# Kernel tuning notes

Measured on AMD Instinct MI355X. Metric: run time of the kernel, lower is better.

## Reference

```python
import jax, jax.numpy as jnp
import numpy as np
import math

B, S, H = 4, 1024, 1024
NH, DH = 16, 64  # MULTI_HEAD, HIDDEN_SIZE_HEAD


def setup_inputs() -> dict:
    key = jax.random.key(0)
    ks = jax.random.split(key, 14)
    w = lambda k: (jax.random.normal(k, (H, H), dtype=jnp.float32) * 0.02)
    b = lambda k: (jax.random.normal(k, (H,), dtype=jnp.float32) * 0.02)
    return {
        "v": jax.random.normal(ks[0], (B, S, H), dtype=jnp.float32),
        "k": jax.random.normal(ks[1], (B, S, H), dtype=jnp.float32),
        "q": jax.random.normal(ks[2], (B, S, H), dtype=jnp.float32),
        "mask": jax.random.randint(ks[3], (B, 1, 1, S), 0, 2) == 1,
        "group_prob": jax.random.uniform(ks[4], (B, S, S), dtype=jnp.float32),
        "Wq": w(ks[5]), "bq": b(ks[6]),
        "Wk": w(ks[7]), "bk": b(ks[8]),
        "Wv": w(ks[9]), "bv": b(ks[10]),
        "Wm": w(ks[11]), "bm": b(ks[12]),
    }


def reference(v, k, q, mask, group_prob, Wq, bq, Wk, bk, Wv, bv, Wm, bm):
    nb = q.shape[0]
    inv_sqrt_dk = 1.0 / math.sqrt(DH)

    def proj(x, W, b):
        # torch Linear: x @ W.T + b, then split heads -> [B, NH, S, DH]
        y = jnp.einsum('bsh,oh->bso', x, W) + b
        return y.reshape(nb, -1, NH, DH).transpose(0, 2, 1, 3)

    qh = proj(q, Wq, bq)
    kh = proj(k, Wk, bk)
    vh = proj(v, Wv, bv)

    scores = jnp.einsum('bhqd,bhkd->bhqk', qh, kh) * inv_sqrt_dk
    scores = jnp.where(mask, jnp.float32(-1e9), scores)
    att = jax.nn.softmax(scores, axis=-1)
    # post-softmax group-prior scaling (the non-standard part)
    att = att * group_prob[:, None, :, :]
    # dropout in eval mode = identity
    out = jnp.einsum('bhqk,bhkd->bhqd', att, vh)
    out = out.transpose(0, 2, 1, 3).reshape(nb, -1, H)
    return jnp.einsum('bsh,oh->bso', out, Wm) + bm
```

## Files before the change

### kernel.cpp

```cpp
#include <hip/hip_runtime.h>

#define S_LEN 1024
#define NHEAD 16
#define DHEAD 64

typedef _Float16 half8 __attribute__((ext_vector_type(8)));
typedef _Float16 half4v __attribute__((ext_vector_type(4)));
typedef float floatx4 __attribute__((ext_vector_type(4)));

#define QSCALE 0.125f
#define EXPSHIFT 4.0f

__device__ __forceinline__ void gll16(const _Float16* g, _Float16* s) {
    __builtin_amdgcn_global_load_lds(
        (const __attribute__((address_space(1))) void*)g,
        (__attribute__((address_space(3))) void*)s, 16, 0, 0);
}

struct SplitArgs {
    const float* src[7];
    _Float16* hi[7];
    int nblk[7];
};

__global__ __launch_bounds__(256) void split_all_kernel(SplitArgs a)
{
    int blk = blockIdx.x, seg = 0, off = 0;
    while (blk >= off + a.nblk[seg]) { off += a.nblk[seg]; ++seg; }
    const int base = (blk - off) * 4096 + threadIdx.x * 4;
#pragma unroll
    for (int u = 0; u < 4; ++u) {
        const int i = base + u * 1024;
        float4 v = *(const float4*)&a.src[seg][i];
        half4v h;
        h.x = (_Float16)v.x; h.y = (_Float16)v.y;
        h.z = (_Float16)v.z; h.w = (_Float16)v.w;
        *(half4v*)&a.hi[seg][i] = h;
    }
}

__global__ __launch_bounds__(256) void gp_prep_kernel(
    const float* __restrict__ gp, _Float16* __restrict__ gpt)
{
    __shared__ _Float16 G[128 * 64];
    const int t = threadIdx.x;
    const int tile = blockIdx.x;
    const int kt = tile & 15, qt = (tile >> 4) & 7, b = tile >> 7;
    const float* src = gp + ((size_t)(b * S_LEN + qt * 128)) * S_LEN + kt * 64;

#pragma unroll
    for (int it = 0; it < 8; ++it) {
        const int idx = it * 256 + t;
        const int q = idx >> 4, kk = (idx & 15) * 4;
        float4 v = *(const float4*)&src[(size_t)q * S_LEN + kk];
        half4v h;
        h.x = (_Float16)v.x; h.y = (_Float16)v.y;
        h.z = (_Float16)v.z; h.w = (_Float16)v.w;
        *(half4v*)&G[q * 64 + kk] = h;
    }
    __syncthreads();

    _Float16* dst = gpt + (size_t)tile * 8192;
#pragma unroll
    for (int ph = 0; ph < 4; ++ph) {
        const int chunk = ph * 256 + t;
        const int l = chunk & 63;
        const int rest = chunk >> 6;
        const int h2 = rest & 1, mt = (rest >> 1) & 1, w = rest >> 2;
        const int qb = w * 32 + mt * 16 + (l >> 4) * 4;
        const int kb = l & 15;
        half8 o;
#pragma unroll
        for (int jj = 0; jj < 2; ++jj)
#pragma unroll
            for (int rg = 0; rg < 4; ++rg)
                o[jj * 4 + rg] = G[(qb + rg) * 64 + kb + (h2 * 2 + jj) * 16];
        *(half8*)&dst[chunk * 8] = o;
    }
}

struct ProjArgs {
    const _Float16* A[3];
    const _Float16* B[3];
    const float* bias[3];
    _Float16* C[3];
};

__global__ __launch_bounds__(256, 3) void proj_gemm_kernel(ProjArgs p)
{
    __shared__ __align__(16) _Float16 Ab[128 * 64];
    __shared__ __align__(16) _Float16 Bb[128 * 64];

    const int bid = blockIdx.x;
    const int xcd = bid & 7;
    const int slot = bid >> 3;
    const int mg = slot & 3;
    const int bx = (slot >> 2) & 7;
    const int z  = slot >> 5;
    const int by = xcd + mg * 8;

    const _Float16* A = p.A[z];
    const _Float16* B = p.B[z];
    const float* bias = p.bias[z];
    _Float16* C = p.C[z];

    const int t = threadIdx.x;
    const int w = t >> 6;
    const int l = t & 63;
    const int r = l & 15;
    const int quad = l >> 4;
    const int k7 = r & 7;
    const int rr = l >> 3, ii = l & 7;
    const int wm = (w >> 1) * 64, wn = (w & 1) * 64;
    const int m0 = by * 128;
    const int n0 = bx * 128;

    floatx4 acc[4][4];
#pragma unroll
    for (int i = 0; i < 4; ++i)
#pragma unroll
        for (int j = 0; j < 4; ++j) acc[i][j] = (floatx4){0.f, 0.f, 0.f, 0.f};

    const _Float16* ssrc = (w < 2) ? A : B;
    _Float16* sdst = (w < 2) ? Ab : Bb;
    const int srow0 = (w < 2) ? m0 : n0;
    const int w01 = w & 1;

    auto stage = [&](int kt) {
        const int k0 = kt * 64;
#pragma unroll
        for (int c = 0; c < 8; ++c) {
            const int R = w01 * 64 + c * 8 + rr;
            const int j = ii ^ (R & 7);
            gll16(ssrc + (size_t)(srow0 + R) * 1024 + k0 + j * 8,
                  sdst + R * 64 + ii * 8);
        }
    };

    stage(0);
    for (int kt = 0; kt < 16; ++kt) {
        __syncthreads();

        half8 ah[4][2], bh[4][2];
#pragma unroll
        for (int i = 0; i < 4; ++i) {
            const int R = wm + i * 16 + r;
            ah[i][0] = *(const half8*)&Ab[R * 64 + ((quad ^ k7) << 3)];
            ah[i][1] = *(const half8*)&Ab[R * 64 + (((4 | quad) ^ k7) << 3)];
        }
#pragma unroll
        for (int j = 0; j < 4; ++j) {
            const int R = wn + j * 16 + r;
            bh[j][0] = *(const half8*)&Bb[R * 64 + ((quad ^ k7) << 3)];
            bh[j][1] = *(const half8*)&Bb[R * 64 + (((4 | quad) ^ k7) << 3)];
        }
        __syncthreads();

        if (kt + 1 < 16) stage(kt + 1);

#pragma unroll
        for (int c = 0; c < 2; ++c)
#pragma unroll
            for (int i = 0; i < 4; ++i)
#pragma unroll
                for (int j = 0; j < 4; ++j)
                    acc[i][j] = __builtin_amdgcn_mfma_f32_16x16x32_f16(
                        ah[i][c], bh[j][c], acc[i][j], 0, 0, 0);
    }

#pragma unroll
    for (int i = 0; i < 4; ++i)
#pragma unroll
        for (int j = 0; j < 4; ++j) {
            const int n = n0 + wn + j * 16 + r;
            const float bv = bias[n];
#pragma unroll
            for (int reg = 0; reg < 4; ++reg) {
                const int m = m0 + wm + i * 16 + quad * 4 + reg;
                float val = acc[i][j][reg] + bv;
                if (z == 0) val *= QSCALE;
                const int b = m >> 10, s = m & 1023;
                const int h = n >> 6, d = n & 63;
                const size_t idx = (z == 2)
                    ? (((size_t)(b * NHEAD + h)) * DHEAD + d) * S_LEN + s
                    : (((size_t)(b * NHEAD + h)) * S_LEN + s) * DHEAD + d;
                C[idx] = (_Float16)val;
            }
        }
}

__global__ __launch_bounds__(256, 2) void out_gemm_kernel(
    const _Float16* __restrict__ A, const _Float16* __restrict__ B,
    const float* __restrict__ bias, float* __restrict__ C)
{
    __shared__ __align__(16) _Float16 Ab[128 * 64];
    __shared__ __align__(16) _Float16 Bb[64 * 64];

    const int bid = blockIdx.x;
    const int xcd = bid & 7;
    const int slot = bid >> 3;
    const int by = xcd + (slot & 3) * 8;
    const int bx = slot >> 2;

    const int t = threadIdx.x;
    const int w = t >> 6;
    const int l = t & 63;
    const int r = l & 15;
    const int quad = l >> 4;
    const int k7 = r & 7;
    const int rr = l >> 3, ii = l & 7;
    const int m0 = by * 128, n0 = bx * 64;

    floatx4 acc[2][4];
#pragma unroll
    for (int mt = 0; mt < 2; ++mt)
#pragma unroll
        for (int j = 0; j < 4; ++j) acc[mt][j] = (floatx4){0.f, 0.f, 0.f, 0.f};

    auto stage = [&](int kt) {
        const int k0 = kt * 64;
        if (w < 2) {
#pragma unroll
            for (int c = 0; c < 8; ++c) {
                const int R = (w & 1) * 64 + c * 8 + rr;
                const int j = ii ^ (R & 7);
                gll16(A + (size_t)(m0 + R) * 1024 + k0 + j * 8,
                      Ab + R * 64 + ii * 8);
            }
        } else {
#pragma unroll
            for (int c = 0; c < 4; ++c) {
                const int R = (w - 2) * 32 + c * 8 + rr;
                const int j = ii ^ (R & 7);
                gll16(B + (size_t)(n0 + R) * 1024 + k0 + j * 8,
                      Bb + R * 64 + ii * 8);
            }
        }
    };

    stage(0);
    for (int kt = 0; kt < 16; ++kt) {
        __syncthreads();

        half8 ah[2][2], bh[4][2];
#pragma unroll
        for (int mt = 0; mt < 2; ++mt) {
            const int R = w * 32 + mt * 16 + r;
            ah[mt][0] = *(const half8*)&Ab[R * 64 + ((quad ^ k7) << 3)];
            ah[mt][1] = *(const half8*)&Ab[R * 64 + (((4 | quad) ^ k7) << 3)];
        }
#pragma unroll
        for (int j = 0; j < 4; ++j) {
            const int R = j * 16 + r;
            bh[j][0] = *(const half8*)&Bb[R * 64 + ((quad ^ k7) << 3)];
            bh[j][1] = *(const half8*)&Bb[R * 64 + (((4 | quad) ^ k7) << 3)];
        }
        __syncthreads();

        if (kt + 1 < 16) stage(kt + 1);

#pragma unroll
        for (int c = 0; c < 2; ++c)
#pragma unroll
            for (int mt = 0; mt < 2; ++mt)
#pragma unroll
                for (int j = 0; j < 4; ++j)
                    acc[mt][j] = __builtin_amdgcn_mfma_f32_16x16x32_f16(
                        ah[mt][c], bh[j][c], acc[mt][j], 0, 0, 0);
    }

#pragma unroll
    for (int mt = 0; mt < 2; ++mt)
#pragma unroll
        for (int j = 0; j < 4; ++j) {
            const int n = n0 + j * 16 + r;
            const float bv = bias[n];
#pragma unroll
            for (int reg = 0; reg < 4; ++reg) {
                const int m = m0 + w * 32 + mt * 16 + quad * 4 + reg;
                C[(size_t)m * 1024 + n] = acc[mt][j][reg] + bv;
            }
        }
}

__global__ __launch_bounds__(256, 2) void attention_mfma_kernel(
    const _Float16* __restrict__ Qhi, const _Float16* __restrict__ Khi,
    const _Float16* __restrict__ Vthi, const _Float16* __restrict__ gpt,
    const int* __restrict__ mask, _Float16* __restrict__ OutHi)
{
    __shared__ __align__(16) _Float16 KhS[2][4096];
    __shared__ __align__(16) _Float16 VhS[2][4096];
    __shared__ __align__(16) _Float16 PS[8192];
    __shared__ int maskS[1024];

    const int t = threadIdx.x;
    const int w = t >> 6;
    const int l = t & 63;
    const int lr = l & 15;
    const int quad = l >> 4;
    const int rr = l >> 3;
    const int ii = l & 7;

    const int h  = blockIdx.x & 15;
    const int qt = (blockIdx.x >> 4) & 7;
    const int b  = blockIdx.x >> 7;
    const int q0 = qt * 128;
    const size_t hb = (size_t)(b * NHEAD + h) * (S_LEN * DHEAD);
    const _Float16* gptile = gpt + (size_t)((b * 8 + qt) * 16) * 8192;

    ((int4*)maskS)[t] = ((const int4*)(mask + (size_t)b * S_LEN))[t];

    half8 qfh[2][2];
#pragma unroll
    for (int mt = 0; mt < 2; ++mt)
#pragma unroll
        for (int c = 0; c < 2; ++c) {
            const size_t off = hb + (size_t)(q0 + w * 32 + mt * 16 + lr) * 64 + c * 32 + quad * 8;
            qfh[mt][c] = *(const half8*)&Qhi[off];
        }

    float lpart[2][4];
    floatx4 Oa[2][4];
#pragma unroll
    for (int mt = 0; mt < 2; ++mt)
#pragma unroll
        for (int rg = 0; rg < 4; ++rg) {
            lpart[mt][rg] = 0.0f;
            Oa[mt][rg] = (floatx4){0.f, 0.f, 0.f, 0.f};
        }

    auto stageK = [&](int kt, int bf) {
        const int k0n = kt * 64;
#pragma unroll
        for (int c2 = 0; c2 < 2; ++c2) {
            const int c = w * 2 + c2;
            const int row = c * 8 + rr;
            const int j = ii ^ (row & 7);
            gll16(Khi + hb + (size_t)(k0n + row) * 64 + j * 8,
                  &KhS[bf][0] + c * 512 + l * 8);
        }
    };
    auto stageV = [&](int kt, int bf) {
        const int k0n = kt * 64;
#pragma unroll
        for (int c2 = 0; c2 < 2; ++c2) {
            const int i = w * 2 + c2;
            const int row = i * 8 + rr;
            const int j = ii ^ (row & 7);
            gll16(Vthi + hb + (size_t)row * S_LEN + k0n + j * 8,
                  &VhS[bf][0] + i * 512 + l * 8);
        }
    };
    auto loadG = [&](half8 (&g)[2][2], int kt) {
#pragma unroll
        for (int mt = 0; mt < 2; ++mt)
#pragma unroll
            for (int h2 = 0; h2 < 2; ++h2)
                g[mt][h2] = *(const half8*)&gptile[(size_t)kt * 8192 +
                    (((w * 2 + mt) * 2 + h2) * 64 + l) * 8];
    };

    half8 gc[2][2], gn[2][2];
    stageK(0, 0);
    stageV(0, 0);
    loadG(gc, 0);
    __syncthreads();

    for (int kt = 0; kt < 16; ++kt) {
        const int bf = kt & 1;
        const int k0 = kt * 64;

        if (kt + 1 < 16) {
            stageK(kt + 1, bf ^ 1);
            stageV(kt + 1, bf ^ 1);
            loadG(gn, kt + 1);
        }

        int mk[4];
#pragma unroll
        for (int j = 0; j < 4; ++j) mk[j] = maskS[k0 + j * 16 + lr];

        floatx4 sc[2][4];
#pragma unroll
        for (int mt = 0; mt < 2; ++mt)
#pragma unroll
            for (int j = 0; j < 4; ++j) sc[mt][j] = (floatx4){0.f, 0.f, 0.f, 0.f};

#pragma unroll
        for (int j = 0; j < 4; ++j) {
            const int key = j * 16 + lr;
            const int base = key * 64;
            const int k7a = key & 7;
            const half8 kh0 = *(const half8*)&KhS[bf][base + (quad ^ k7a) * 8];
            const half8 kh1 = *(const half8*)&KhS[bf][base + ((4 + quad) ^ k7a) * 8];
#pragma unroll
            for (int mt = 0; mt < 2; ++mt) {
                floatx4 a = sc[mt][j];
                a = __builtin_amdgcn_mfma_f32_16x16x32_f16(qfh[mt][0], kh0, a, 0, 0, 0);
                a = __builtin_amdgcn_mfma_f32_16x16x32_f16(qfh[mt][1], kh1, a, 0, 0, 0);
                sc[mt][j] = a;
            }
        }

#pragma unroll
        for (int mt = 0; mt < 2; ++mt) {
            const half8 g0 = gc[mt][0];
            const half8 g1 = gc[mt][1];
            const int qlb = w * 32 + mt * 16 + quad * 4;
#pragma unroll
            for (int j = 0; j < 4; ++j) {
                const int col = j * 16 + lr;
                const int cc = col >> 3, wi = col & 7;
#pragma unroll
                for (int rg = 0; rg < 4; ++rg) {
                    const float p = mk[j] ? 0.0f : __expf(sc[mt][j][rg] - EXPSHIFT);
                    lpart[mt][rg] += p;
                    const float g = (float)((j < 2) ? g0[(j & 1) * 4 + rg]
                                                    : g1[(j & 1) * 4 + rg]);
                    const int qloc = qlb + rg;
                    PS[qloc * 64 + (cc ^ (qloc & 7)) * 8 + wi] = (_Float16)(p * g);
                }
            }
        }

        half8 pf[2][2];
#pragma unroll
        for (int mt = 0; mt < 2; ++mt) {
            const int qloc = w * 32 + mt * 16 + lr;
            const int q7 = qloc & 7;
            pf[mt][0] = *(const half8*)&PS[qloc * 64 + (quad ^ q7) * 8];
            pf[mt][1] = *(const half8*)&PS[qloc * 64 + ((4 + quad) ^ q7) * 8];
        }
#pragma unroll
        for (int dt = 0; dt < 4; ++dt) {
            const int d = dt * 16 + lr;
            const int base = d * 64, d7 = d & 7;
            const half8 vh0 = *(const half8*)&VhS[bf][base + (quad ^ d7) * 8];
            const half8 vh1 = *(const half8*)&VhS[bf][base + ((4 + quad) ^ d7) * 8];
#pragma unroll
            for (int mt = 0; mt < 2; ++mt) {
                floatx4 a = Oa[mt][dt];
                a = __builtin_amdgcn_mfma_f32_16x16x32_f16(pf[mt][0], vh0, a, 0, 0, 0);
                a = __builtin_amdgcn_mfma_f32_16x16x32_f16(pf[mt][1], vh1, a, 0, 0, 0);
                Oa[mt][dt] = a;
            }
        }

        __syncthreads();

        if (kt + 1 < 16) {
#pragma unroll
            for (int mt = 0; mt < 2; ++mt)
#pragma unroll
                for (int h2 = 0; h2 < 2; ++h2) gc[mt][h2] = gn[mt][h2];
        }
    }

#pragma unroll
    for (int mt = 0; mt < 2; ++mt)
#pragma unroll
        for (int rg = 0; rg < 4; ++rg) {
#pragma unroll
            for (int off = 1; off < 16; off <<= 1)
                lpart[mt][rg] += __shfl_xor(lpart[mt][rg], off, 64);
        }

#pragma unroll
    for (int mt = 0; mt < 2; ++mt)
#pragma unroll
        for (int rg = 0; rg < 4; ++rg) {
            const int s = q0 + w * 32 + mt * 16 + quad * 4 + rg;
            const float linv = 1.0f / lpart[mt][rg];
#pragma unroll
            for (int dt = 0; dt < 4; ++dt) {
                const float val = Oa[mt][dt][rg] * linv;
                const size_t idx = ((size_t)(b * S_LEN + s)) * 1024 + h * 64 + dt * 16 + lr;
                OutHi[idx] = (_Float16)val;
            }
        }
}

extern "C" void kernel_launch(void* const* d_in, const int* in_sizes, int n_in,
                              void* d_out, int out_size, void* d_ws, size_t ws_size,
                              hipStream_t stream) {
    const float* v    = (const float*)d_in[0];
    const float* k    = (const float*)d_in[1];
    const float* q    = (const float*)d_in[2];
    const int*   mask = (const int*)d_in[3];
    const float* gp   = (const float*)d_in[4];
    const float* Wq   = (const float*)d_in[5];
    const float* bq   = (const float*)d_in[6];
    const float* Wk   = (const float*)d_in[7];
    const float* bk   = (const float*)d_in[8];
    const float* Wv   = (const float*)d_in[9];
    const float* bv   = (const float*)d_in[10];
    const float* Wm   = (const float*)d_in[11];
    const float* bm   = (const float*)d_in[12];
    float* out = (float*)d_out;

    uint8_t* w8 = (uint8_t*)d_ws;
    const size_t MB = 1024 * 1024;
    _Float16* q_h  = (_Float16*)(w8 + 0 * MB);
    _Float16* k_h  = (_Float16*)(w8 + 8 * MB);
    _Float16* v_h  = (_Float16*)(w8 + 16 * MB);
    _Float16* Wq_h = (_Float16*)(w8 + 24 * MB);
    _Float16* Wk_h = (_Float16*)(w8 + 26 * MB);
    _Float16* Wv_h = (_Float16*)(w8 + 28 * MB);
    _Float16* Wm_h = (_Float16*)(w8 + 30 * MB);
    _Float16* Qh   = (_Float16*)(w8 + 32 * MB);
    _Float16* Kh   = (_Float16*)(w8 + 40 * MB);
    _Float16* Vt   = (_Float16*)(w8 + 48 * MB);
    _Float16* gpt  = (_Float16*)(w8 + 56 * MB);
    _Float16* at   = (_Float16*)(w8 + 0 * MB);

    SplitArgs sa;
    sa.src[0] = q;  sa.hi[0] = q_h;  sa.nblk[0] = 1024;
    sa.src[1] = k;  sa.hi[1] = k_h;  sa.nblk[1] = 1024;
    sa.src[2] = v;  sa.hi[2] = v_h;  sa.nblk[2] = 1024;
    sa.src[3] = Wq; sa.hi[3] = Wq_h; sa.nblk[3] = 256;
    sa.src[4] = Wk; sa.hi[4] = Wk_h; sa.nblk[4] = 256;
    sa.src[5] = Wv; sa.hi[5] = Wv_h; sa.nblk[5] = 256;
    sa.src[6] = Wm; sa.hi[6] = Wm_h; sa.nblk[6] = 256;
    split_all_kernel<<<4096, 256, 0, stream>>>(sa);

    gp_prep_kernel<<<512, 256, 0, stream>>>(gp, gpt);

    ProjArgs pa;
    pa.A[0] = q_h; pa.B[0] = Wq_h; pa.bias[0] = bq; pa.C[0] = Qh;
    pa.A[1] = k_h; pa.B[1] = Wk_h; pa.bias[1] = bk; pa.C[1] = Kh;
    pa.A[2] = v_h; pa.B[2] = Wv_h; pa.bias[2] = bv; pa.C[2] = Vt;
    proj_gemm_kernel<<<768, 256, 0, stream>>>(pa);

    attention_mfma_kernel<<<512, 256, 0, stream>>>(
        Qh, Kh, Vt, gpt, mask, at);

    out_gemm_kernel<<<512, 256, 0, stream>>>(
        at, Wm_h, bm, out);
}
```

Before: 229.5 us.

## Halve attention query tile to 64 rows and double grid for occupancy

Each attention block now handles 64 query rows (16 per wave) instead of 128, with the grid doubled to 1024 blocks and launch bounds raised to 4 blocks per SM. The P staging buffer is halved and the mask LDS cache is dropped in favour of direct global reads. The group-prior multiply is now done in fp16. The aim is more resident waves and less register and LDS pressure per block. The cost is that K and V tiles are staged twice as often per query row, so each loaded tile is reused less.

```diff
diff --git a/kernel.cpp b/kernel.cpp
--- a/kernel.cpp
+++ b/kernel.cpp
@@ -283,15 +283,14 @@
         }
 }
 
-__global__ __launch_bounds__(256, 2) void attention_mfma_kernel(
+__global__ __launch_bounds__(256, 4) void attention_mfma_kernel(
     const _Float16* __restrict__ Qhi, const _Float16* __restrict__ Khi,
     const _Float16* __restrict__ Vthi, const _Float16* __restrict__ gpt,
     const int* __restrict__ mask, _Float16* __restrict__ OutHi)
 {
     __shared__ __align__(16) _Float16 KhS[2][4096];
     __shared__ __align__(16) _Float16 VhS[2][4096];
-    __shared__ __align__(16) _Float16 PS[8192];
-    __shared__ int maskS[1024];
+    __shared__ __align__(16) _Float16 PS[4096];
 
     const int t = threadIdx.x;
     const int w = t >> 6;
@@ -301,33 +300,29 @@
     const int rr = l >> 3;
     const int ii = l & 7;
 
-    const int h  = blockIdx.x & 15;
-    const int qt = (blockIdx.x >> 4) & 7;
-    const int b  = blockIdx.x >> 7;
-    const int q0 = qt * 128;
+    const int h   = blockIdx.x & 15;
+    const int qt2 = (blockIdx.x >> 4) & 15;
+    const int b   = blockIdx.x >> 8;
+    const int q0  = qt2 * 64;
     const size_t hb = (size_t)(b * NHEAD + h) * (S_LEN * DHEAD);
-    const _Float16* gptile = gpt + (size_t)((b * 8 + qt) * 16) * 8192;
-
-    ((int4*)maskS)[t] = ((const int4*)(mask + (size_t)b * S_LEN))[t];
-
-    half8 qfh[2][2];
-#pragma unroll
-    for (int mt = 0; mt < 2; ++mt)
-#pragma unroll
-        for (int c = 0; c < 2; ++c) {
-            const size_t off = hb + (size_t)(q0 + w * 32 + mt * 16 + lr) * 64 + c * 32 + quad * 8;
-            qfh[mt][c] = *(const half8*)&Qhi[off];
-        }
-
-    float lpart[2][4];
-    floatx4 Oa[2][4];
-#pragma unroll
-    for (int mt = 0; mt < 2; ++mt)
-#pragma unroll
-        for (int rg = 0; rg < 4; ++rg) {
-            lpart[mt][rg] = 0.0f;
-            Oa[mt][rg] = (floatx4){0.f, 0.f, 0.f, 0.f};
-        }
+    const _Float16* gptile = gpt + (size_t)((b * 8 + (qt2 >> 1)) * 16) * 8192;
+    const int wold = (qt2 & 1) * 2 + (w >> 1);
+    const int mtold = w & 1;
+
+    half8 qfh[2];
+#pragma unroll
+    for (int c = 0; c < 2; ++c) {
+        const size_t off = hb + (size_t)(q0 + w * 16 + lr) * 64 + c * 32 + quad * 8;
+        qfh[c] = *(const half8*)&Qhi[off];
+    }
+
+    float lpart[4];
+    floatx4 Oa[4];
+#pragma unroll
+    for (int rg = 0; rg < 4; ++rg) {
+        lpart[rg] = 0.0f;
+        Oa[rg] = (floatx4){0.f, 0.f, 0.f, 0.f};
+    }
 
     auto stageK = [&](int kt, int bf) {
         const int k0n = kt * 64;
@@ -351,16 +346,14 @@
                   &VhS[bf][0] + i * 512 + l * 8);
         }
     };
-    auto loadG = [&](half8 (&g)[2][2], int kt) {
-#pragma unroll
-        for (int mt = 0; mt < 2; ++mt)
-#pragma unroll
-            for (int h2 = 0; h2 < 2; ++h2)
-                g[mt][h2] = *(const half8*)&gptile[(size_t)kt * 8192 +
-                    (((w * 2 + mt) * 2 + h2) * 64 + l) * 8];
+    auto loadG = [&](half8 (&g)[2], int kt) {
+#pragma unroll
+        for (int h2 = 0; h2 < 2; ++h2)
+            g[h2] = *(const half8*)&gptile[(size_t)kt * 8192 +
+                (((wold * 2 + mtold) * 2 + h2) * 64 + l) * 8];
     };
 
-    half8 gc[2][2], gn[2][2];
+    half8 gc[2], gn[2];
     stageK(0, 0);
     stageV(0, 0);
     loadG(gc, 0);
@@ -378,13 +371,11 @@
 
         int mk[4];
 #pragma unroll
-        for (int j = 0; j < 4; ++j) mk[j] = maskS[k0 + j * 16 + lr];
-
-        floatx4 sc[2][4];
-#pragma unroll
-        for (int mt = 0; mt < 2; ++mt)
-#pragma unroll
-            for (int j = 0; j < 4; ++j) sc[mt][j] = (floatx4){0.f, 0.f, 0.f, 0.f};
+        for (int j = 0; j < 4; ++j) mk[j] = mask[b * S_LEN + k0 + j * 16 + lr];
+
+        floatx4 sc[4];
+#pragma unroll
+        for (int j = 0; j < 4; ++j) sc[j] = (floatx4){0.f, 0.f, 0.f, 0.f};
 
 #pragma unroll
         for (int j = 0; j < 4; ++j) {
@@ -393,43 +384,37 @@
             const int k7a = key & 7;
             const half8 kh0 = *(const half8*)&KhS[bf][base + (quad ^ k7a) * 8];
             const half8 kh1 = *(const half8*)&KhS[bf][base + ((4 + quad) ^ k7a) * 8];
-#pragma unroll
-            for (int mt = 0; mt < 2; ++mt) {
-                floatx4 a = sc[mt][j];
-                a = __builtin_amdgcn_mfma_f32_16x16x32_f16(qfh[mt][0], kh0, a, 0, 0, 0);
-                a = __builtin_amdgcn_mfma_f32_16x16x32_f16(qfh[mt][1], kh1, a, 0, 0, 0);
-                sc[mt][j] = a;
-            }
-        }
-
-#pragma unroll
-        for (int mt = 0; mt < 2; ++mt) {
-            const half8 g0 = gc[mt][0];
-            const half8 g1 = gc[mt][1];
-            const int qlb = w * 32 + mt * 16 + quad * 4;
+            floatx4 a = sc[j];
+            a = __builtin_amdgcn_mfma_f32_16x16x32_f16(qfh[0], kh0, a, 0, 0, 0);
+            a = __builtin_amdgcn_mfma_f32_16x16x32_f16(qfh[1], kh1, a, 0, 0, 0);
+            sc[j] = a;
+        }
+
+        {
+            const int qlb = w * 16 + quad * 4;
 #pragma unroll
             for (int j = 0; j < 4; ++j) {
                 const int col = j * 16 + lr;
                 const int cc = col >> 3, wi = col & 7;
+                const half8 g = (j < 2) ? gc[0] : gc[1];
 #pragma unroll
                 for (int rg = 0; rg < 4; ++rg) {
-                    const float p = mk[j] ? 0.0f : __expf(sc[mt][j][rg] - EXPSHIFT);
-                    lpart[mt][rg] += p;
-                    const float g = (float)((j < 2) ? g0[(j & 1) * 4 + rg]
-                                                    : g1[(j & 1) * 4 + rg]);
+                    const float e = __expf(sc[j][rg] - EXPSHIFT);
+                    const float p = mk[j] ? 0.0f : e;
+                    lpart[rg] += p;
+                    const _Float16 res = (_Float16)p * g[(j & 1) * 4 + rg];
                     const int qloc = qlb + rg;
-                    PS[qloc * 64 + (cc ^ (qloc & 7)) * 8 + wi] = (_Float16)(p * g);
+                    PS[qloc * 64 + (cc ^ (qloc & 7)) * 8 + wi] = res;
                 }
             }
         }
 
-        half8 pf[2][2];
-#pragma unroll
-        for (int mt = 0; mt < 2; ++mt) {
-            const int qloc = w * 32 + mt * 16 + lr;
+        half8 pf[2];
+        {
+            const int qloc = w * 16 + lr;
             const int q7 = qloc & 7;
-            pf[mt][0] = *(const half8*)&PS[qloc * 64 + (quad ^ q7) * 8];
-            pf[mt][1] = *(const half8*)&PS[qloc * 64 + ((4 + quad) ^ q7) * 8];
+            pf[0] = *(const half8*)&PS[qloc * 64 + (quad ^ q7) * 8];
+            pf[1] = *(const half8*)&PS[qloc * 64 + ((4 + quad) ^ q7) * 8];
         }
 #pragma unroll
         for (int dt = 0; dt < 4; ++dt) {
@@ -437,47 +422,38 @@
             const int base = d * 64, d7 = d & 7;
             const half8 vh0 = *(const half8*)&VhS[bf][base + (quad ^ d7) * 8];
             const half8 vh1 = *(const half8*)&VhS[bf][base + ((4 + quad) ^ d7) * 8];
-#pragma unroll
-            for (int mt = 0; mt < 2; ++mt) {
-                floatx4 a = Oa[mt][dt];
-                a = __builtin_amdgcn_mfma_f32_16x16x32_f16(pf[mt][0], vh0, a, 0, 0, 0);
-                a = __builtin_amdgcn_mfma_f32_16x16x32_f16(pf[mt][1], vh1, a, 0, 0, 0);
-                Oa[mt][dt] = a;
-            }
+            floatx4 a = Oa[dt];
+            a = __builtin_amdgcn_mfma_f32_16x16x32_f16(pf[0], vh0, a, 0, 0, 0);
+            a = __builtin_amdgcn_mfma_f32_16x16x32_f16(pf[1], vh1, a, 0, 0, 0);
+            Oa[dt] = a;
         }
 
         __syncthreads();
 
         if (kt + 1 < 16) {
 #pragma unroll
-            for (int mt = 0; mt < 2; ++mt)
-#pragma unroll
-                for (int h2 = 0; h2 < 2; ++h2) gc[mt][h2] = gn[mt][h2];
-        }
-    }
-
-#pragma unroll
-    for (int mt = 0; mt < 2; ++mt)
-#pragma unroll
-        for (int rg = 0; rg < 4; ++rg) {
-#pragma unroll
-            for (int off = 1; off < 16; off <<= 1)
-                lpart[mt][rg] += __shfl_xor(lpart[mt][rg], off, 64);
-        }
-
-#pragma unroll
-    for (int mt = 0; mt < 2; ++mt)
-#pragma unroll
-        for (int rg = 0; rg < 4; ++rg) {
-            const int s = q0 + w * 32 + mt * 16 + quad * 4 + rg;
-            const float linv = 1.0f / lpart[mt][rg];
-#pragma unroll
-            for (int dt = 0; dt < 4; ++dt) {
-                const float val = Oa[mt][dt][rg] * linv;
-                const size_t idx = ((size_t)(b * S_LEN + s)) * 1024 + h * 64 + dt * 16 + lr;
-                OutHi[idx] = (_Float16)val;
-            }
-        }
+            for (int h2 = 0; h2 < 2; ++h2) gc[h2] = gn[h2];
+        }
+    }
+
+#pragma unroll
+    for (int rg = 0; rg < 4; ++rg) {
+#pragma unroll
+        for (int off = 1; off < 16; off <<= 1)
+            lpart[rg] += __shfl_xor(lpart[rg], off, 64);
+    }
+
+#pragma unroll
+    for (int rg = 0; rg < 4; ++rg) {
+        const int s = q0 + w * 16 + quad * 4 + rg;
+        const float linv = 1.0f / lpart[rg];
+#pragma unroll
+        for (int dt = 0; dt < 4; ++dt) {
+            const float val = Oa[dt][rg] * linv;
+            const size_t idx = ((size_t)(b * S_LEN + s)) * 1024 + h * 64 + dt * 16 + lr;
+            OutHi[idx] = (_Float16)val;
+        }
+    }
 }
 
 extern "C" void kernel_launch(void* const* d_in, const int* in_sizes, int n_in,
@@ -531,7 +507,7 @@
     pa.A[2] = v_h; pa.B[2] = Wv_h; pa.bias[2] = bv; pa.C[2] = Vt;
     proj_gemm_kernel<<<768, 256, 0, stream>>>(pa);
 
-    attention_mfma_kernel<<<512, 256, 0, stream>>>(
+    attention_mfma_kernel<<<1024, 256, 0, stream>>>(
         Qh, Kh, Vt, gpt, mask, at);
 
     out_gemm_kernel<<<512, 256, 0, stream>>>(
```

New measurement: 232.3 us. About the same (+1.2%).
